# Kernel tuning notes

Measured on AMD Instinct MI355X. Metric: run time of the kernel, lower is better.

Reference implementation:

```python
import jax, jax.numpy as jnp
import numpy as np

N_A, N_C, N_L = 50000, 10000, 10000
HID = 128


def _gatv2(x_src, x_dst, src, dst, ea, Wl, bl, Wr, br, We, att, bias, H):
    # GATv2Conv (PyG) bipartite, edge_dim=1, concat=False (mean over heads), eval mode (no dropout)
    C = bias.shape[0]
    n_dst = x_dst.shape[0]
    xl = (x_src @ Wl + bl).reshape(-1, H, C)      # [N_src, H, C]
    xr = (x_dst @ Wr + br).reshape(-1, H, C)      # [N_dst, H, C]
    e = jax.nn.leaky_relu(xl[src] + xr[dst] + (ea @ We).reshape(-1, H, C), 0.2)  # [E,H,C]
    logit = jnp.einsum('ehc,hc->eh', e, att)      # [E,H]
    m = jax.ops.segment_max(logit, dst, num_segments=n_dst)
    m = jax.lax.stop_gradient(jnp.where(jnp.isfinite(m), m, 0.0))
    ex = jnp.exp(logit - m[dst])
    denom = jax.ops.segment_sum(ex, dst, num_segments=n_dst)
    alpha = ex / (denom[dst] + 1e-16)             # segment softmax over incoming edges
    out = jax.ops.segment_sum(alpha[:, :, None] * xl[src], dst, num_segments=n_dst)
    return out.mean(axis=1) + bias                # concat=False -> head mean + bias


def setup_inputs() -> dict:
    key = jax.random.key(0)
    ks = iter(jax.random.split(key, 80))
    def rn(shape, s=1.0):
        return jax.random.normal(next(ks), shape, jnp.float32) * s
    inp = {}
    inp['x_asset'] = rn((N_A, 512))
    inp['x_creator'] = rn((N_C, 2))
    inp['x_licensee'] = rn((N_L, 1))
    # edges: (name, E, src_max, dst_max)
    edges = [('cb', 50000, N_A, N_C), ('lt', 100000, N_A, N_L), ('sim', 200000, N_A, N_A),
             ('fw', 100000, N_A, N_A), ('rcb', 50000, N_C, N_A), ('rlt', 100000, N_L, N_A)]
    for name, E, smax, dmax in edges:
        inp[f'{name}_src'] = jax.random.randint(next(ks), (E,), 0, smax, jnp.int32)
        inp[f'{name}_dst'] = jax.random.randint(next(ks), (E,), 0, dmax, jnp.int32)
        inp[f'ea_{name}'] = rn((E, 1))
    w = 0.05  # param scale
    inp['Wp_a'] = rn((512, HID), w); inp['bp_a'] = rn((HID,), w)
    inp['Wp_c'] = rn((2, HID), w);   inp['bp_c'] = rn((HID,), w)
    inp['Wp_l'] = rn((1, HID), w);   inp['bp_l'] = rn((HID,), w)
    # layer 1: heads=2, stacked over the 6 relations
    H1 = 2
    inp['Wl1'] = rn((6, HID, H1 * HID), w); inp['bl1'] = rn((6, H1 * HID), w)
    inp['Wr1'] = rn((6, HID, H1 * HID), w); inp['br1'] = rn((6, H1 * HID), w)
    inp['We1'] = rn((6, 1, H1 * HID), w)
    inp['att1'] = rn((6, H1, HID), w); inp['bias1'] = rn((6, HID), w)
    # layer 2: heads=1
    inp['Wl2'] = rn((6, HID, HID), w); inp['bl2'] = rn((6, HID), w)
    inp['Wr2'] = rn((6, HID, HID), w); inp['br2'] = rn((6, HID), w)
    inp['We2'] = rn((6, 1, HID), w)
    inp['att2'] = rn((6, 1, HID), w); inp['bias2'] = rn((6, HID), w)
    inp['Wc1'] = rn((HID, HID), w); inp['bc1'] = rn((HID,), w)
    inp['Wc2'] = rn((HID, 3), w);   inp['bc2'] = rn((3,), w)
    inp['query_asset_index'] = 123
    return inp


def reference(x_asset, x_creator, x_licensee, Wp_a, bp_a, Wp_c, bp_c, Wp_l, bp_l,
              Wl1, bl1, Wr1, br1, We1, att1, bias1,
              Wl2, bl2, Wr2, br2, We2, att2, bias2,
              Wc1, bc1, Wc2, bc2,
              ea_cb, ea_lt, ea_sim, ea_fw, ea_rcb, ea_rlt,
              cb_src, cb_dst, lt_src, lt_dst, sim_src, sim_dst,
              fw_src, fw_dst, rcb_src, rcb_dst, rlt_src, rlt_dst,
              query_asset_index):
    x = {'Asset': x_asset @ Wp_a + bp_a,
         'Creator': x_creator @ Wp_c + bp_c,
         'Licensee': x_licensee @ Wp_l + bp_l}
    rels = [('Asset', 'Creator', cb_src, cb_dst, ea_cb),
            ('Asset', 'Licensee', lt_src, lt_dst, ea_lt),
            ('Asset', 'Asset', sim_src, sim_dst, ea_sim),
            ('Asset', 'Asset', fw_src, fw_dst, ea_fw),
            ('Creator', 'Asset', rcb_src, rcb_dst, ea_rcb),
            ('Licensee', 'Asset', rlt_src, rlt_dst, ea_rlt)]

    def hetero_layer(x, Wl, bl, Wr, br, We, att, bias, H):
        out = {k: jnp.zeros((v.shape[0], HID), v.dtype) for k, v in x.items()}
        for i, (st, dt, s, d, ea) in enumerate(rels):  # HeteroConv aggr='sum'
            out[dt] = out[dt] + _gatv2(x[st], x[dt], s, d, ea,
                                       Wl[i], bl[i], Wr[i], br[i], We[i], att[i], bias[i], H)
        return out

    x = hetero_layer(x, Wl1, bl1, Wr1, br1, We1, att1, bias1, 2)
    x = {k: jax.nn.relu(v) for k, v in x.items()}  # eval: dropout is identity
    x = hetero_layer(x, Wl2, bl2, Wr2, br2, We2, att2, bias2, 1)
    x = {k: jax.nn.relu(v) for k, v in x.items()}
    a = x['Asset'][query_asset_index]
    return jax.nn.relu(a @ Wc1 + bc1) @ Wc2 + bc2
```

## Files before the change

kernel.cpp:

```cpp
#include <hip/hip_runtime.h>
#include <math.h>

#define FAMAX 64
#define FCMAX 32
#define FLMAX 32
#define N1MAX 512
#define N2MAX 128
#define DMAX  128

struct Inputs {
  const float *x_asset, *x_creator, *x_licensee;
  const float *Wp_a,*bp_a,*Wp_c,*bp_c,*Wp_l,*bp_l;
  const float *Wl1,*bl1,*Wr1,*br1,*We1,*att1,*bias1;
  const float *Wl2,*bl2,*Wr2,*br2,*We2,*att2,*bias2;
  const float *Wc1,*bc1,*Wc2,*bc2;
};

struct Edges {
  const int *cb_s,*cb_d;  const float* ea_cb;  int Ecb;
  const int *lt_s,*lt_d;  const float* ea_lt;  int Elt;
  const int *sim_s,*sim_d;const float* ea_sim; int Esim;
  const int *fw_s,*fw_d;  const float* ea_fw;  int Efw;
  const int *rcb_s,*rcb_d;const float* ea_rcb; int Ercb;
  const int *rlt_s,*rlt_d;const float* ea_rlt; int Erlt;
};

struct WSP {
  int* cnt;
  int *dfA,*dfC,*dfL;
  int *fa,*fc,*fl;
  int* l2rel; int* l2src; float* l2ea;
  int* l1rel; int* l1src; int* l1dslot; float* l1ea;
  float *xr1a,*xr1c,*xr1l;
  float* xl1e;
  float *x1a,*x1c,*x1l;
  float* xl2e;
  float* logit2;
};

__device__ __forceinline__ float leaky(float x){ return x > 0.f ? x : 0.2f*x; }

__device__ __forceinline__ void claim(int* flag, int* cnt, int* list, int node, int cap){
  int old = atomicCAS(&flag[node], 0, 1);
  if (old == 0){
    int k = atomicAdd(cnt, 1);
    if (k < cap){ list[k] = node; atomicExch(&flag[node], k + 2); }
    else atomicExch(&flag[node], 0);
  }
}

__device__ __forceinline__ void proj256(int type, int node, const Inputs& in,
                                        float* h0, float* xs, float* part){
  int t = threadIdx.x;
  if (type == 0){
    xs[t]       = in.x_asset[(size_t)node*512 + t];
    xs[t + 256] = in.x_asset[(size_t)node*512 + t + 256];
    __syncthreads();
    int j = t & 127, g2 = t >> 7;
    float acc = 0.f;
    const float* W = in.Wp_a + (size_t)g2*256*128 + j;
    const float* xg = xs + g2*256;
    for (int k=0;k<256;k++) acc = fmaf(xg[k], W[(size_t)k*128], acc);
    part[t] = acc;
    __syncthreads();
    if (t < 128) h0[t] = in.bp_a[t] + part[t] + part[128 + t];
  } else if (type == 1){
    if (t < 128)
      h0[t] = in.bp_c[t] + in.x_creator[node*2]*in.Wp_c[t]
            + in.x_creator[node*2+1]*in.Wp_c[128+t];
  } else {
    if (t < 128)
      h0[t] = in.bp_l[t] + in.x_licensee[node]*in.Wp_l[t];
  }
  __syncthreads();
}

__global__ void k1_scan_l2(Edges eg, const int* qptr, WSP w){
  int q = qptr[0];
  if (blockIdx.x==0 && threadIdx.x==0) claim(w.dfA, &w.cnt[1], w.fa, q, FAMAX);
  int total = eg.Esim + eg.Efw + eg.Ercb + eg.Erlt;
  for (int i = blockIdx.x*blockDim.x + threadIdx.x; i < total; i += gridDim.x*blockDim.x){
    int j = i, rel; const int *sp,*dp; const float* ep;
    if (j < eg.Esim){ rel=2; sp=eg.sim_s; dp=eg.sim_d; ep=eg.ea_sim; }
    else { j -= eg.Esim;
      if (j < eg.Efw){ rel=3; sp=eg.fw_s; dp=eg.fw_d; ep=eg.ea_fw; }
      else { j -= eg.Efw;
        if (j < eg.Ercb){ rel=4; sp=eg.rcb_s; dp=eg.rcb_d; ep=eg.ea_rcb; }
        else { j -= eg.Ercb; rel=5; sp=eg.rlt_s; dp=eg.rlt_d; ep=eg.ea_rlt; }
      }
    }
    if (dp[j] == q){
      int src = sp[j];
      int k = atomicAdd(&w.cnt[0], 1);
      if (k < N2MAX){ w.l2rel[k]=rel; w.l2src[k]=src; w.l2ea[k]=ep[j]; }
      if (rel <= 3) claim(w.dfA,&w.cnt[1],w.fa,src,FAMAX);
      else if (rel == 4) claim(w.dfC,&w.cnt[2],w.fc,src,FCMAX);
      else claim(w.dfL,&w.cnt[3],w.fl,src,FLMAX);
    }
  }
}

__global__ void k2_scan_l1(Edges eg, WSP w){
  int total = eg.Ecb+eg.Elt+eg.Esim+eg.Efw+eg.Ercb+eg.Erlt;
  for (int i = blockIdx.x*blockDim.x + threadIdx.x; i < total; i += gridDim.x*blockDim.x){
    int j = i, rel; const int *sp,*dp; const float* ep; const int* flag;
    if (j < eg.Ecb){ rel=0; sp=eg.cb_s; dp=eg.cb_d; ep=eg.ea_cb; flag=w.dfC; }
    else { j -= eg.Ecb;
    if (j < eg.Elt){ rel=1; sp=eg.lt_s; dp=eg.lt_d; ep=eg.ea_lt; flag=w.dfL; }
    else { j -= eg.Elt;
    if (j < eg.Esim){ rel=2; sp=eg.sim_s; dp=eg.sim_d; ep=eg.ea_sim; flag=w.dfA; }
    else { j -= eg.Esim;
    if (j < eg.Efw){ rel=3; sp=eg.fw_s; dp=eg.fw_d; ep=eg.ea_fw; flag=w.dfA; }
    else { j -= eg.Efw;
    if (j < eg.Ercb){ rel=4; sp=eg.rcb_s; dp=eg.rcb_d; ep=eg.ea_rcb; flag=w.dfA; }
    else { j -= eg.Ercb; rel=5; sp=eg.rlt_s; dp=eg.rlt_d; ep=eg.ea_rlt; flag=w.dfA; }}}}}
    int f = flag[dp[j]];
    if (f >= 2){
      int k = atomicAdd(&w.cnt[4], 1);
      if (k < N1MAX){ w.l1rel[k]=rel; w.l1src[k]=sp[j]; w.l1dslot[k]=f-2; w.l1ea[k]=ep[j]; }
    }
  }
}

__global__ void k3_fused(Inputs in, WSP w){
  __shared__ float xs[512];
  __shared__ float part[256];
  __shared__ float h0[128];
  int b = blockIdx.x, t = threadIdx.x;
  int nfa = w.cnt[1] < FAMAX ? w.cnt[1] : FAMAX;
  int nfc = w.cnt[2] < FCMAX ? w.cnt[2] : FCMAX;
  int nfl = w.cnt[3] < FLMAX ? w.cnt[3] : FLMAX;
  if (b < FAMAX){
    if (b >= nfa) return;
    proj256(0, w.fa[b], in, h0, xs, part);
    for (int ridx=0; ridx<4; ridx++){
      int rel = 2 + ridx;
      float acc = in.br1[rel*256 + t];
      const float* W = in.Wr1 + (size_t)rel*128*256 + t;
      for (int c=0;c<128;c++) acc = fmaf(h0[c], W[(size_t)c*256], acc);
      w.xr1a[((size_t)b*4 + ridx)*256 + t] = acc;
    }
  } else if (b < FAMAX + FCMAX){
    int slot = b - FAMAX;
    if (slot >= nfc) return;
    proj256(1, w.fc[slot], in, h0, xs, part);
    float acc = in.br1[0*256 + t];
    const float* W = in.Wr1 + t;
    for (int c=0;c<128;c++) acc = fmaf(h0[c], W[(size_t)c*256], acc);
    w.xr1c[(size_t)slot*256 + t] = acc;
  } else if (b < FAMAX + FCMAX + FLMAX){
    int slot = b - FAMAX - FCMAX;
    if (slot >= nfl) return;
    proj256(2, w.fl[slot], in, h0, xs, part);
    float acc = in.br1[1*256 + t];
    const float* W = in.Wr1 + (size_t)1*128*256 + t;
    for (int c=0;c<128;c++) acc = fmaf(h0[c], W[(size_t)c*256], acc);
    w.xr1l[(size_t)slot*256 + t] = acc;
  } else {
    int i = b - (FAMAX + FCMAX + FLMAX);
    int n1 = w.cnt[4] < N1MAX ? w.cnt[4] : N1MAX;
    if (i >= n1) return;
    int rel = w.l1rel[i], src = w.l1src[i];
    int stype = (rel <= 3) ? 0 : (rel == 4 ? 1 : 2);
    proj256(stype, src, in, h0, xs, part);
    float acc = in.bl1[rel*256 + t];
    const float* W = in.Wl1 + (size_t)rel*128*256 + t;
    for (int c=0;c<128;c++) acc = fmaf(h0[c], W[(size_t)c*256], acc);
    w.xl1e[(size_t)i*256 + t] = acc;
  }
}

__global__ void k4_agg(Inputs in, WSP w){
  __shared__ float red[256];
  __shared__ int   lrel[N1MAX];
  __shared__ int   lslot[N1MAX];
  __shared__ float lea[N1MAX];
  __shared__ float lg[DMAX][2];
  __shared__ int   eid[DMAX];
  int b = blockIdx.x, t = threadIdx.x;
  int nfa = w.cnt[1] < FAMAX ? w.cnt[1] : FAMAX;
  int nfc = w.cnt[2] < FCMAX ? w.cnt[2] : FCMAX;
  int nfl = w.cnt[3] < FLMAX ? w.cnt[3] : FLMAX;
  int type, slot;
  if (b < FAMAX){ slot=b; if (slot>=nfa) return; type=0; }
  else if (b < FAMAX+FCMAX){ slot=b-FAMAX; if (slot>=nfc) return; type=1; }
  else { slot=b-FAMAX-FCMAX; if (slot>=nfl) return; type=2; }
  int n1 = w.cnt[4] < N1MAX ? w.cnt[4] : N1MAX;
  for (int i = t; i < n1; i += 256){
    lrel[i] = w.l1rel[i]; lslot[i] = w.l1dslot[i]; lea[i] = w.l1ea[i];
  }
  __syncthreads();
  int h = t >> 7, c = t & 127;
  float out = 0.f;
  int r0, r1;
  if (type==0){ r0=2; r1=5; } else if (type==1){ r0=0; r1=0; } else { r0=1; r1=1; }
  for (int r=r0; r<=r1; r++){
    if (t < 128) out += in.bias1[r*128 + t];
    const float* xrp;
    if (r >= 2) xrp = w.xr1a + ((size_t)slot*4 + (r-2))*256;
    else if (r == 0) xrp = w.xr1c + (size_t)slot*256;
    else xrp = w.xr1l + (size_t)slot*256;
    float xrv = xrp[t];
    float wev = in.We1[r*256 + t];
    float atv = in.att1[(r*2 + h)*128 + c];
    int nd = 0;
    for (int i=0;i<n1 && nd<DMAX;i++){
      if (lrel[i]==r && lslot[i]==slot){
        float e = leaky(w.xl1e[(size_t)i*256 + t] + xrv + lea[i]*wev);
        red[t] = e * atv;
        __syncthreads();
        for (int s=64; s>0; s>>=1){ if (c < s) red[t] += red[t+s]; __syncthreads(); }
        if (t == 0){ lg[nd][0] = red[0]; lg[nd][1] = red[128]; eid[nd] = i; }
        __syncthreads();
        nd++;
      }
    }
    if (nd == 0) continue;
    float m0=-INFINITY, m1=-INFINITY;
    for (int d=0; d<nd; d++){ m0 = fmaxf(m0, lg[d][0]); m1 = fmaxf(m1, lg[d][1]); }
    float d0=0.f, d1=0.f;
    for (int d=0; d<nd; d++){ d0 += expf(lg[d][0]-m0); d1 += expf(lg[d][1]-m1); }
    if (t < 128){
      float a0=0.f, a1=0.f;
      for (int d=0; d<nd; d++){
        int i = eid[d];
        a0 = fmaf(expf(lg[d][0]-m0), w.xl1e[(size_t)i*256 + t],       a0);
        a1 = fmaf(expf(lg[d][1]-m1), w.xl1e[(size_t)i*256 + 128 + t], a1);
      }
      out += 0.5f*(a0/(d0+1e-16f) + a1/(d1+1e-16f));
    }
    __syncthreads();
  }
  if (t < 128){
    float v = fmaxf(out, 0.f);
    if (type==0) w.x1a[slot*128 + t] = v;
    else if (type==1) w.x1c[slot*128 + t] = v;
    else w.x1l[slot*128 + t] = v;
  }
}

__global__ void k5b_l2edge(Inputs in, WSP w, const int* qptr){
  __shared__ float xq[128];
  __shared__ float xsrc[128];
  __shared__ float red[128];
  int i = blockIdx.x, j = threadIdx.x;
  int n2 = w.cnt[0] < N2MAX ? w.cnt[0] : N2MAX;
  if (i >= n2) return;
  int rel = w.l2rel[i], src = w.l2src[i];
  float ea = w.l2ea[i];
  int f; const float* xb;
  if (rel <= 3){ f = w.dfA[src]; xb = w.x1a; }
  else if (rel == 4){ f = w.dfC[src]; xb = w.x1c; }
  else { f = w.dfL[src]; xb = w.x1l; }
  if (f < 2){
    w.xl2e[(size_t)i*128 + j] = 0.f;
    if (j == 0) w.logit2[i] = -INFINITY;
    return;
  }
  int q = qptr[0];
  int qs = w.dfA[q] - 2;
  xq[j]   = w.x1a[(size_t)qs*128 + j];
  xsrc[j] = xb[(size_t)(f-2)*128 + j];
  __syncthreads();
  float xr2 = in.br2[rel*128 + j];
  {
    const float* W = in.Wr2 + (size_t)rel*128*128 + j;
    for (int c=0;c<128;c++) xr2 = fmaf(xq[c], W[(size_t)c*128], xr2);
  }
  float xl2 = in.bl2[rel*128 + j];
  {
    const float* W = in.Wl2 + (size_t)rel*128*128 + j;
    for (int c=0;c<128;c++) xl2 = fmaf(xsrc[c], W[(size_t)c*128], xl2);
  }
  w.xl2e[(size_t)i*128 + j] = xl2;
  float e = leaky(xl2 + xr2 + ea*in.We2[rel*128 + j]);
  red[j] = e * in.att2[rel*128 + j];
  __syncthreads();
  for (int s=64; s>0; s>>=1){ if (j < s) red[j] += red[j+s]; __syncthreads(); }
  if (j == 0) w.logit2[i] = red[0];
}

__global__ void k5c_final(Inputs in, WSP w, float* outp){
  __shared__ float x2[128];
  __shared__ float tt[128];
  int j = threadIdx.x;
  int n2 = w.cnt[0] < N2MAX ? w.cnt[0] : N2MAX;
  float o = 0.f;
  for (int r=2; r<=5; r++){
    o += in.bias2[r*128 + j];
    float m = -INFINITY;
    for (int i=0;i<n2;i++) if (w.l2rel[i]==r) m = fmaxf(m, w.logit2[i]);
    if (m == -INFINITY) continue;
    float d = 0.f, acc = 0.f;
    for (int i=0;i<n2;i++) if (w.l2rel[i]==r){
      float e = expf(w.logit2[i] - m);
      d += e;
      acc = fmaf(e, w.xl2e[(size_t)i*128 + j], acc);
    }
    o += acc/(d + 1e-16f);
  }
  x2[j] = fmaxf(o, 0.f);
  __syncthreads();
  float acc = in.bc1[j];
  for (int c=0;c<128;c++) acc = fmaf(x2[c], in.Wc1[c*128 + j], acc);
  tt[j] = fmaxf(acc, 0.f);
  __syncthreads();
  if (j < 3){
    float r = in.bc2[j];
    for (int c=0;c<128;c++) r = fmaf(tt[c], in.Wc2[c*3 + j], r);
    outp[j] = r;
  }
}

extern "C" void kernel_launch(void* const* d_in, const int* in_sizes, int n_in,
                              void* d_out, int out_size, void* d_ws, size_t ws_size,
                              hipStream_t stream){
  Inputs in;
  in.x_asset   = (const float*)d_in[0];
  in.x_creator = (const float*)d_in[1];
  in.x_licensee= (const float*)d_in[2];
  Edges eg;
  eg.cb_s =(const int*)d_in[3];  eg.cb_d =(const int*)d_in[4];  eg.ea_cb =(const float*)d_in[5];  eg.Ecb = in_sizes[3];
  eg.lt_s =(const int*)d_in[6];  eg.lt_d =(const int*)d_in[7];  eg.ea_lt =(const float*)d_in[8];  eg.Elt = in_sizes[6];
  eg.sim_s=(const int*)d_in[9];  eg.sim_d=(const int*)d_in[10]; eg.ea_sim=(const float*)d_in[11]; eg.Esim= in_sizes[9];
  eg.fw_s =(const int*)d_in[12]; eg.fw_d =(const int*)d_in[13]; eg.ea_fw =(const float*)d_in[14]; eg.Efw = in_sizes[12];
  eg.rcb_s=(const int*)d_in[15]; eg.rcb_d=(const int*)d_in[16]; eg.ea_rcb=(const float*)d_in[17]; eg.Ercb= in_sizes[15];
  eg.rlt_s=(const int*)d_in[18]; eg.rlt_d=(const int*)d_in[19]; eg.ea_rlt=(const float*)d_in[20]; eg.Erlt= in_sizes[18];
  in.Wp_a=(const float*)d_in[21]; in.bp_a=(const float*)d_in[22];
  in.Wp_c=(const float*)d_in[23]; in.bp_c=(const float*)d_in[24];
  in.Wp_l=(const float*)d_in[25]; in.bp_l=(const float*)d_in[26];
  in.Wl1=(const float*)d_in[27]; in.bl1=(const float*)d_in[28];
  in.Wr1=(const float*)d_in[29]; in.br1=(const float*)d_in[30];
  in.We1=(const float*)d_in[31]; in.att1=(const float*)d_in[32]; in.bias1=(const float*)d_in[33];
  in.Wl2=(const float*)d_in[34]; in.bl2=(const float*)d_in[35];
  in.Wr2=(const float*)d_in[36]; in.br2=(const float*)d_in[37];
  in.We2=(const float*)d_in[38]; in.att2=(const float*)d_in[39]; in.bias2=(const float*)d_in[40];
  in.Wc1=(const float*)d_in[41]; in.bc1=(const float*)d_in[42];
  in.Wc2=(const float*)d_in[43]; in.bc2=(const float*)d_in[44];
  const int* qptr = (const int*)d_in[45];

  char* p = (char*)d_ws;
  auto carve = [&](size_t n)->char*{ char* r = p; p += ((n + 255) & ~(size_t)255); return r; };
  WSP w;
  w.cnt  = (int*)carve(16*4);
  w.dfA  = (int*)carve(50000*4); w.dfC = (int*)carve(10000*4); w.dfL = (int*)carve(10000*4);
  size_t zero_bytes = (size_t)(p - (char*)d_ws);
  w.fa = (int*)carve(FAMAX*4); w.fc = (int*)carve(FCMAX*4); w.fl = (int*)carve(FLMAX*4);
  w.l2rel=(int*)carve(N2MAX*4); w.l2src=(int*)carve(N2MAX*4); w.l2ea=(float*)carve(N2MAX*4);
  w.l1rel=(int*)carve(N1MAX*4); w.l1src=(int*)carve(N1MAX*4); w.l1dslot=(int*)carve(N1MAX*4); w.l1ea=(float*)carve(N1MAX*4);
  w.xr1a=(float*)carve((size_t)FAMAX*4*256*4);
  w.xr1c=(float*)carve((size_t)FCMAX*256*4);
  w.xr1l=(float*)carve((size_t)FLMAX*256*4);
  w.xl1e=(float*)carve((size_t)N1MAX*256*4);
  w.x1a=(float*)carve((size_t)FAMAX*128*4);
  w.x1c=(float*)carve((size_t)FCMAX*128*4);
  w.x1l=(float*)carve((size_t)FLMAX*128*4);
  w.xl2e=(float*)carve((size_t)N2MAX*128*4);
  w.logit2=(float*)carve(N2MAX*4);

  hipMemsetAsync(d_ws, 0, zero_bytes, stream);

  int tE2 = eg.Esim + eg.Efw + eg.Ercb + eg.Erlt;
  k1_scan_l2<<<(tE2+255)/256, 256, 0, stream>>>(eg, qptr, w);
  int tE1 = eg.Ecb + eg.Elt + tE2;
  k2_scan_l1<<<(tE1+255)/256, 256, 0, stream>>>(eg, w);
  k3_fused<<<FAMAX + FCMAX + FLMAX + N1MAX, 256, 0, stream>>>(in, w);
  k4_agg<<<FAMAX + FCMAX + FLMAX, 256, 0, stream>>>(in, w);
  k5b_l2edge<<<N2MAX, 128, 0, stream>>>(in, w, qptr);
  k5c_final<<<1, 128, 0, stream>>>(in, w, (float*)d_out);
}
```

Measured before the change: 315.3 us.

## Compute layer-1 edge logits per edge block instead of serial per-destination loop

The layer-1 attention logits are now computed inside the per-edge projection kernel. Each edge block also recomputes the destination node's projection and right-side transform, and writes the two head logits to a new buffer. The aggregation kernel then only reads the precomputed logits and does the softmax-weighted sum with 128 threads and no barriers. This removes the serial per-edge reductions with repeated __syncthreads in k4, at the cost of recomputing destination projections once per edge.

```diff
diff --git a/kernel.cpp b/kernel.cpp
--- a/kernel.cpp
+++ b/kernel.cpp
@@ -6,7 +6,6 @@
 #define FLMAX 32
 #define N1MAX 512
 #define N2MAX 128
-#define DMAX  128
 
 struct Inputs {
   const float *x_asset, *x_creator, *x_licensee;
@@ -31,8 +30,8 @@
   int *fa,*fc,*fl;
   int* l2rel; int* l2src; float* l2ea;
   int* l1rel; int* l1src; int* l1dslot; float* l1ea;
-  float *xr1a,*xr1c,*xr1l;
   float* xl1e;
+  float* logit1;
   float *x1a,*x1c,*x1l;
   float* xl2e;
   float* logit2;
@@ -122,62 +121,43 @@
   }
 }
 
-__global__ void k3_fused(Inputs in, WSP w){
+__global__ void k3_edge(Inputs in, WSP w){
   __shared__ float xs[512];
   __shared__ float part[256];
-  __shared__ float h0[128];
-  int b = blockIdx.x, t = threadIdx.x;
-  int nfa = w.cnt[1] < FAMAX ? w.cnt[1] : FAMAX;
-  int nfc = w.cnt[2] < FCMAX ? w.cnt[2] : FCMAX;
-  int nfl = w.cnt[3] < FLMAX ? w.cnt[3] : FLMAX;
-  if (b < FAMAX){
-    if (b >= nfa) return;
-    proj256(0, w.fa[b], in, h0, xs, part);
-    for (int ridx=0; ridx<4; ridx++){
-      int rel = 2 + ridx;
-      float acc = in.br1[rel*256 + t];
-      const float* W = in.Wr1 + (size_t)rel*128*256 + t;
-      for (int c=0;c<128;c++) acc = fmaf(h0[c], W[(size_t)c*256], acc);
-      w.xr1a[((size_t)b*4 + ridx)*256 + t] = acc;
-    }
-  } else if (b < FAMAX + FCMAX){
-    int slot = b - FAMAX;
-    if (slot >= nfc) return;
-    proj256(1, w.fc[slot], in, h0, xs, part);
-    float acc = in.br1[0*256 + t];
-    const float* W = in.Wr1 + t;
-    for (int c=0;c<128;c++) acc = fmaf(h0[c], W[(size_t)c*256], acc);
-    w.xr1c[(size_t)slot*256 + t] = acc;
-  } else if (b < FAMAX + FCMAX + FLMAX){
-    int slot = b - FAMAX - FCMAX;
-    if (slot >= nfl) return;
-    proj256(2, w.fl[slot], in, h0, xs, part);
-    float acc = in.br1[1*256 + t];
-    const float* W = in.Wr1 + (size_t)1*128*256 + t;
-    for (int c=0;c<128;c++) acc = fmaf(h0[c], W[(size_t)c*256], acc);
-    w.xr1l[(size_t)slot*256 + t] = acc;
-  } else {
-    int i = b - (FAMAX + FCMAX + FLMAX);
-    int n1 = w.cnt[4] < N1MAX ? w.cnt[4] : N1MAX;
-    if (i >= n1) return;
-    int rel = w.l1rel[i], src = w.l1src[i];
-    int stype = (rel <= 3) ? 0 : (rel == 4 ? 1 : 2);
-    proj256(stype, src, in, h0, xs, part);
-    float acc = in.bl1[rel*256 + t];
+  __shared__ float h0s[128];
+  __shared__ float h0d[128];
+  __shared__ float red[256];
+  int i = blockIdx.x, t = threadIdx.x;
+  int n1 = w.cnt[4] < N1MAX ? w.cnt[4] : N1MAX;
+  if (i >= n1) return;
+  int rel = w.l1rel[i], src = w.l1src[i], dslot = w.l1dslot[i];
+  float ea = w.l1ea[i];
+  int stype = (rel <= 3) ? 0 : (rel == 4 ? 1 : 2);
+  int dtype = (rel == 0) ? 1 : (rel == 1 ? 2 : 0);
+  int dnode = (rel == 0) ? w.fc[dslot] : (rel == 1 ? w.fl[dslot] : w.fa[dslot]);
+  proj256(stype, src, in, h0s, xs, part);
+  float xl1 = in.bl1[rel*256 + t];
+  {
     const float* W = in.Wl1 + (size_t)rel*128*256 + t;
-    for (int c=0;c<128;c++) acc = fmaf(h0[c], W[(size_t)c*256], acc);
-    w.xl1e[(size_t)i*256 + t] = acc;
-  }
+    for (int c=0;c<128;c++) xl1 = fmaf(h0s[c], W[(size_t)c*256], xl1);
+  }
+  w.xl1e[(size_t)i*256 + t] = xl1;
+  proj256(dtype, dnode, in, h0d, xs, part);
+  float xr1 = in.br1[rel*256 + t];
+  {
+    const float* W = in.Wr1 + (size_t)rel*128*256 + t;
+    for (int c=0;c<128;c++) xr1 = fmaf(h0d[c], W[(size_t)c*256], xr1);
+  }
+  int h = t >> 7, c = t & 127;
+  float e = leaky(xl1 + xr1 + ea*in.We1[rel*256 + t]);
+  red[t] = e * in.att1[(rel*2 + h)*128 + c];
+  __syncthreads();
+  for (int s=64; s>0; s>>=1){ if (c < s) red[t] += red[t+s]; __syncthreads(); }
+  if (c == 0) w.logit1[i*2 + h] = red[t];
 }
 
 __global__ void k4_agg(Inputs in, WSP w){
-  __shared__ float red[256];
-  __shared__ int   lrel[N1MAX];
-  __shared__ int   lslot[N1MAX];
-  __shared__ float lea[N1MAX];
-  __shared__ float lg[DMAX][2];
-  __shared__ int   eid[DMAX];
-  int b = blockIdx.x, t = threadIdx.x;
+  int b = blockIdx.x, j = threadIdx.x;
   int nfa = w.cnt[1] < FAMAX ? w.cnt[1] : FAMAX;
   int nfc = w.cnt[2] < FCMAX ? w.cnt[2] : FCMAX;
   int nfl = w.cnt[3] < FLMAX ? w.cnt[3] : FLMAX;
@@ -186,57 +166,35 @@
   else if (b < FAMAX+FCMAX){ slot=b-FAMAX; if (slot>=nfc) return; type=1; }
   else { slot=b-FAMAX-FCMAX; if (slot>=nfl) return; type=2; }
   int n1 = w.cnt[4] < N1MAX ? w.cnt[4] : N1MAX;
-  for (int i = t; i < n1; i += 256){
-    lrel[i] = w.l1rel[i]; lslot[i] = w.l1dslot[i]; lea[i] = w.l1ea[i];
-  }
-  __syncthreads();
-  int h = t >> 7, c = t & 127;
   float out = 0.f;
   int r0, r1;
   if (type==0){ r0=2; r1=5; } else if (type==1){ r0=0; r1=0; } else { r0=1; r1=1; }
   for (int r=r0; r<=r1; r++){
-    if (t < 128) out += in.bias1[r*128 + t];
-    const float* xrp;
-    if (r >= 2) xrp = w.xr1a + ((size_t)slot*4 + (r-2))*256;
-    else if (r == 0) xrp = w.xr1c + (size_t)slot*256;
-    else xrp = w.xr1l + (size_t)slot*256;
-    float xrv = xrp[t];
-    float wev = in.We1[r*256 + t];
-    float atv = in.att1[(r*2 + h)*128 + c];
-    int nd = 0;
-    for (int i=0;i<n1 && nd<DMAX;i++){
-      if (lrel[i]==r && lslot[i]==slot){
-        float e = leaky(w.xl1e[(size_t)i*256 + t] + xrv + lea[i]*wev);
-        red[t] = e * atv;
-        __syncthreads();
-        for (int s=64; s>0; s>>=1){ if (c < s) red[t] += red[t+s]; __syncthreads(); }
-        if (t == 0){ lg[nd][0] = red[0]; lg[nd][1] = red[128]; eid[nd] = i; }
-        __syncthreads();
-        nd++;
+    out += in.bias1[r*128 + j];
+    float m0=-INFINITY, m1=-INFINITY;
+    for (int i=0;i<n1;i++){
+      if (w.l1rel[i]==r && w.l1dslot[i]==slot){
+        m0 = fmaxf(m0, w.logit1[i*2]);
+        m1 = fmaxf(m1, w.logit1[i*2+1]);
       }
     }
-    if (nd == 0) continue;
-    float m0=-INFINITY, m1=-INFINITY;
-    for (int d=0; d<nd; d++){ m0 = fmaxf(m0, lg[d][0]); m1 = fmaxf(m1, lg[d][1]); }
-    float d0=0.f, d1=0.f;
-    for (int d=0; d<nd; d++){ d0 += expf(lg[d][0]-m0); d1 += expf(lg[d][1]-m1); }
-    if (t < 128){
-      float a0=0.f, a1=0.f;
-      for (int d=0; d<nd; d++){
-        int i = eid[d];
-        a0 = fmaf(expf(lg[d][0]-m0), w.xl1e[(size_t)i*256 + t],       a0);
-        a1 = fmaf(expf(lg[d][1]-m1), w.xl1e[(size_t)i*256 + 128 + t], a1);
+    if (m0 == -INFINITY) continue;
+    float d0=0.f, d1=0.f, a0=0.f, a1=0.f;
+    for (int i=0;i<n1;i++){
+      if (w.l1rel[i]==r && w.l1dslot[i]==slot){
+        float e0 = expf(w.logit1[i*2]   - m0);
+        float e1 = expf(w.logit1[i*2+1] - m1);
+        d0 += e0; d1 += e1;
+        a0 = fmaf(e0, w.xl1e[(size_t)i*256 + j],       a0);
+        a1 = fmaf(e1, w.xl1e[(size_t)i*256 + 128 + j], a1);
       }
-      out += 0.5f*(a0/(d0+1e-16f) + a1/(d1+1e-16f));
-    }
-    __syncthreads();
-  }
-  if (t < 128){
-    float v = fmaxf(out, 0.f);
-    if (type==0) w.x1a[slot*128 + t] = v;
-    else if (type==1) w.x1c[slot*128 + t] = v;
-    else w.x1l[slot*128 + t] = v;
-  }
+    }
+    out += 0.5f*(a0/(d0+1e-16f) + a1/(d1+1e-16f));
+  }
+  float v = fmaxf(out, 0.f);
+  if (type==0) w.x1a[slot*128 + j] = v;
+  else if (type==1) w.x1c[slot*128 + j] = v;
+  else w.x1l[slot*128 + j] = v;
 }
 
 __global__ void k5b_l2edge(Inputs in, WSP w, const int* qptr){
@@ -348,10 +306,8 @@
   w.fa = (int*)carve(FAMAX*4); w.fc = (int*)carve(FCMAX*4); w.fl = (int*)carve(FLMAX*4);
   w.l2rel=(int*)carve(N2MAX*4); w.l2src=(int*)carve(N2MAX*4); w.l2ea=(float*)carve(N2MAX*4);
   w.l1rel=(int*)carve(N1MAX*4); w.l1src=(int*)carve(N1MAX*4); w.l1dslot=(int*)carve(N1MAX*4); w.l1ea=(float*)carve(N1MAX*4);
-  w.xr1a=(float*)carve((size_t)FAMAX*4*256*4);
-  w.xr1c=(float*)carve((size_t)FCMAX*256*4);
-  w.xr1l=(float*)carve((size_t)FLMAX*256*4);
   w.xl1e=(float*)carve((size_t)N1MAX*256*4);
+  w.logit1=(float*)carve((size_t)N1MAX*2*4);
   w.x1a=(float*)carve((size_t)FAMAX*128*4);
   w.x1c=(float*)carve((size_t)FCMAX*128*4);
   w.x1l=(float*)carve((size_t)FLMAX*128*4);
@@ -364,8 +320,8 @@
   k1_scan_l2<<<(tE2+255)/256, 256, 0, stream>>>(eg, qptr, w);
   int tE1 = eg.Ecb + eg.Elt + tE2;
   k2_scan_l1<<<(tE1+255)/256, 256, 0, stream>>>(eg, w);
-  k3_fused<<<FAMAX + FCMAX + FLMAX + N1MAX, 256, 0, stream>>>(in, w);
-  k4_agg<<<FAMAX + FCMAX + FLMAX, 256, 0, stream>>>(in, w);
+  k3_edge<<<N1MAX, 256, 0, stream>>>(in, w);
+  k4_agg<<<FAMAX + FCMAX + FLMAX, 128, 0, stream>>>(in, w);
   k5b_l2edge<<<N2MAX, 128, 0, stream>>>(in, w, qptr);
   k5c_final<<<1, 128, 0, stream>>>(in, w, (float*)d_out);
 }
```

Measured after the change: 307.1 us. 2.6% less time.
